# Kernel optimization log

Hardware: AMD Instinct MI355X
Metric: run time of the kernel (lower is better)

## Reference

```python
import jax, jax.numpy as jnp
import numpy as np

D_MODEL = 768
NHEAD = 12
HEAD_DIM = D_MODEL // NHEAD
B, L = 8, 1024


def setup_inputs() -> dict:
    key = jax.random.key(0)
    ks = jax.random.split(key, 10)
    s = 0.02  # init scale for weights
    return {
        "x": jax.random.normal(ks[0], (B, L, D_MODEL), dtype=jnp.float32),
        "pos": jax.random.normal(ks[1], (B, L, D_MODEL), dtype=jnp.float32),
        "qkv_w": jax.random.normal(ks[2], (3 * D_MODEL, D_MODEL), dtype=jnp.float32) * s,
        "qkv_b": jnp.zeros((3 * D_MODEL,), dtype=jnp.float32),
        "pq_w": jax.random.normal(ks[3], (D_MODEL, D_MODEL), dtype=jnp.float32) * s,
        "pq_b": jnp.zeros((D_MODEL,), dtype=jnp.float32),
        "pk_w": jax.random.normal(ks[4], (D_MODEL, D_MODEL), dtype=jnp.float32) * s,
        "pk_b": jnp.zeros((D_MODEL,), dtype=jnp.float32),
    }


def reference(x, pos, qkv_w, qkv_b, pq_w, pq_b, pk_w, pk_b):
    b, l, d = x.shape
    h, hd = NHEAD, HEAD_DIM

    qkv = x @ qkv_w.T + qkv_b  # (b, l, 3d)
    q, k, v = jnp.split(qkv, 3, axis=-1)
    # rearrange 'b l (h d) -> b l h d'
    q = q.reshape(b, l, h, hd)
    k = k.reshape(b, l, h, hd)
    v = v.reshape(b, l, h, hd)

    pq = (pos @ pq_w.T + pq_b).reshape(b, l, h, hd)
    pk = (pos @ pk_w.T + pk_b).reshape(b, l, h, hd)

    CC = jnp.einsum('bnhd,blhd->bhnl', q, k)
    CP = jnp.einsum('bnhd,blhd->bhnl', q, pq)
    PC = jnp.einsum('bnhd,blhd->bhnl', k, pk)

    # Faithful to source: only PC is scaled (operator precedence in original)
    scale = (3 * d) ** 0.5
    attn = jax.nn.softmax(CC + CP + PC / scale, axis=-1)

    out = jnp.einsum('bhnl,blhd->bnhd', attn, v)  # (b, n, h, hd)
    return out
```

## Files before the change

### kernel.cpp

```cpp
#include <hip/hip_runtime.h>
#include <hip/hip_bf16.h>

#define NHEAD 12
#define BATCH 8
#define SEQ 1024
#define LOG2E 1.4426950408889634f

typedef __bf16 bf16x8 __attribute__((ext_vector_type(8)));
typedef float  f32x4  __attribute__((ext_vector_type(4)));

#define WAITVM0 asm volatile("s_waitcnt vmcnt(0)" ::: "memory")
#define WAITVM4 asm volatile("s_waitcnt vmcnt(4)" ::: "memory")

#define MFMA(A, B, C) __builtin_amdgcn_mfma_f32_16x16x32_bf16(A, B, C, 0, 0, 0)

__device__ __forceinline__ unsigned short f2bf(float f) {
    union { float f; unsigned u; } v; v.f = f;
    unsigned u = v.u;
    u += 0x7fff + ((u >> 16) & 1);
    return (unsigned short)(u >> 16);
}

__device__ __forceinline__ unsigned pkbf(float a, float b) {
    union { __hip_bfloat162 h; unsigned u; } cv;
    cv.h = __float22bfloat162_rn(make_float2(a, b));
    return cv.u;
}

__device__ __forceinline__ void gload_lds16(const void* g, void* l) {
    __builtin_amdgcn_global_load_lds(
        (const __attribute__((address_space(1))) unsigned*)g,
        (__attribute__((address_space(3))) unsigned*)l, 16, 0, 0);
}

#define SZ_X    6291456
#define SZ_QKVW 1769472
#define SZ_PW   589824
#define CONV_TOTAL 15532032

__global__ __launch_bounds__(256) void convert_kernel(
    const float* __restrict__ x, const float* __restrict__ pos,
    const float* __restrict__ qkv_w, const float* __restrict__ pq_w,
    const float* __restrict__ pk_w, unsigned short* __restrict__ dst)
{
    const size_t i4 = ((size_t)blockIdx.x * 256 + threadIdx.x) * 4;
    if (i4 >= CONV_TOTAL) return;
    const float* src; size_t off;
    if (i4 < SZ_X)                { src = x;     off = i4; }
    else if (i4 < 2 * SZ_X)       { src = pos;   off = i4 - SZ_X; }
    else if (i4 < 2 * SZ_X + SZ_QKVW) { src = qkv_w; off = i4 - 2 * SZ_X; }
    else if (i4 < 2 * SZ_X + SZ_QKVW + SZ_PW) { src = pq_w; off = i4 - 2 * SZ_X - SZ_QKVW; }
    else                          { src = pk_w;  off = i4 - 2 * SZ_X - SZ_QKVW - SZ_PW; }
    float4 v = *(const float4*)(src + off);
    ushort4 o;
    o.x = f2bf(v.x); o.y = f2bf(v.y); o.z = f2bf(v.z); o.w = f2bf(v.w);
    *(ushort4*)(dst + i4) = o;
}


#define PROJ_STAGE(K0, AS, BS) do {                                          \
    const int k0_ = (K0);                                                    \
    const unsigned short* asrc_; int acol_;                                  \
    if (g == 4)                    { asrc_ = posb; acol_ = k0_; }            \
    else if (g == 3 && k0_ >= 768) { asrc_ = posb; acol_ = k0_ - 768; }      \
    else                           { asrc_ = xb;   acol_ = k0_; }            \
    gload_lds16(asrc_ + (size_t)(m0 + r0) * 768 + acol_ + q0 * 8, &AS[base0]);\
    gload_lds16(asrc_ + (size_t)(m0 + r1) * 768 + acol_ + q1 * 8, &AS[base1]);\
    const unsigned short* wsrc_; int wro_, wco_;                             \
    if (g <= 2)       { wsrc_ = qkvw; wro_ = n0;        wco_ = k0_; }        \
    else if (g == 3) {                                                       \
        if (k0_ < 768) { wsrc_ = qkvw; wro_ = n0 - 1536; wco_ = k0_; }       \
        else           { wsrc_ = pqw;  wro_ = n0 - 2304; wco_ = k0_ - 768; } \
    } else            { wsrc_ = pkw;  wro_ = n0 - 3072; wco_ = k0_; }        \
    gload_lds16(wsrc_ + (size_t)(wro_ + r0) * 768 + wco_ + q0 * 8, &BS[base0]);\
    gload_lds16(wsrc_ + (size_t)(wro_ + r1) * 768 + wco_ + q1 * 8, &BS[base1]);\
} while (0)

#define PROJ_COMPUTE(AS, BS) do {                                            \
    bf16x8 af[4], bfr[4];                                                    \
    _Pragma("unroll")                                                        \
    for (int mt = 0; mt < 4; ++mt) {                                         \
        const int rr = wm + mt * 16 + col16;                                 \
        af[mt] = *(const bf16x8*)&AS[rr * 32 + ((quad ^ ((rr >> 1) & 3)) * 8)];\
    }                                                                        \
    _Pragma("unroll")                                                        \
    for (int nt = 0; nt < 4; ++nt) {                                         \
        const int rr = wn + nt * 16 + col16;                                 \
        bfr[nt] = *(const bf16x8*)&BS[rr * 32 + ((quad ^ ((rr >> 1) & 3)) * 8)];\
    }                                                                        \
    _Pragma("unroll")                                                        \
    for (int mt = 0; mt < 4; ++mt)                                           \
        _Pragma("unroll")                                                    \
        for (int nt = 0; nt < 4; ++nt)                                       \
            acc[mt][nt] = MFMA(af[mt], bfr[nt], acc[mt][nt]);                \
} while (0)

__global__ __launch_bounds__(256, 3) void proj_kernel(
    const unsigned short* __restrict__ xb, const unsigned short* __restrict__ posb,
    const unsigned short* __restrict__ qkvw, const unsigned short* __restrict__ pqw,
    const unsigned short* __restrict__ pkw,
    const float* __restrict__ qkv_b, const float* __restrict__ pq_b,
    const float* __restrict__ pk_b,
    unsigned short* __restrict__ Q2, unsigned short* __restrict__ K2,
    unsigned short* __restrict__ Vt, int band)
{
    __shared__ unsigned short As0[128 * 32];
    __shared__ unsigned short As1[128 * 32];
    __shared__ unsigned short As2[128 * 32];
    __shared__ unsigned short Bs0[128 * 32];
    __shared__ unsigned short Bs1[128 * 32];
    __shared__ unsigned short Bs2[128 * 32];

    const int id  = blockIdx.x;
    const int xcd = id & 7;
    const int idx = id >> 3;
    const int nt30 = (idx / band + 18) % 30;
    const int m0 = (xcd * band + idx % band) * 128;
    const int n0 = nt30 * 128;
    const int g  = n0 / 768;
    const int nk = (g == 3) ? 48 : 24;

    const int tid   = threadIdx.x;
    const int lane  = tid & 63;
    const int w     = tid >> 6;
    const int wm    = (w & 1) * 64;
    const int wn    = (w >> 1) * 64;
    const int quad  = lane >> 4;
    const int col16 = lane & 15;

    const int c0 = w * 64 + lane;
    const int c1 = c0 + 256;
    const int r0 = c0 >> 2, q0 = (c0 & 3) ^ ((c0 >> 3) & 3);
    const int r1 = c1 >> 2, q1 = (c1 & 3) ^ ((c1 >> 3) & 3);
    const int base0 = (w * 64) * 8;
    const int base1 = (w * 64 + 256) * 8;

    f32x4 acc[4][4];
    const f32x4 fzero = {0.f, 0.f, 0.f, 0.f};
#pragma unroll
    for (int mt = 0; mt < 4; ++mt)
#pragma unroll
        for (int nt = 0; nt < 4; ++nt) acc[mt][nt] = fzero;

    PROJ_STAGE(0, As0, Bs0);
    PROJ_STAGE(32, As1, Bs1);

    for (int kt = 0; kt < nk; kt += 3) {
        WAITVM4;
        __syncthreads();
        PROJ_STAGE((kt + 2) * 32, As2, Bs2);
        PROJ_COMPUTE(As0, Bs0);

        WAITVM4;
        __syncthreads();
        if (kt + 3 < nk) PROJ_STAGE((kt + 3) * 32, As0, Bs0);
        PROJ_COMPUTE(As1, Bs1);

        if (kt + 3 >= nk) { WAITVM0; } else { WAITVM4; }
        __syncthreads();
        if (kt + 4 < nk) PROJ_STAGE((kt + 4) * 32, As1, Bs1);
        PROJ_COMPUTE(As2, Bs2);
    }

    if (g == 2) {
#pragma unroll
        for (int mt = 0; mt < 4; ++mt) {
            const int mbase = m0 + wm + mt * 16 + quad * 4;
#pragma unroll
            for (int nt = 0; nt < 4; ++nt) {
                const int n = n0 + wn + nt * 16 + col16;
                const int b = mbase >> 10, l0 = mbase & 1023;
                const int c = n - 1536, h = c >> 6, dd = c & 63;
                const float bias = qkv_b[n];
                uint2 pk;
                pk.x = pkbf(acc[mt][nt][0] + bias, acc[mt][nt][1] + bias);
                pk.y = pkbf(acc[mt][nt][2] + bias, acc[mt][nt][3] + bias);
                *(uint2*)&Vt[((size_t)(b * NHEAD + h) * 64 + dd) * 1024 + l0] = pk;
            }
        }
    } else {
#pragma unroll
        for (int p = 0; p < 4; ++p) {
            __syncthreads();
            if ((wm >> 6) == (p >> 1)) {
#pragma unroll
                for (int mth = 0; mth < 2; ++mth) {
                    const int mt = ((p & 1) << 1) | mth;
#pragma unroll
                    for (int nt = 0; nt < 4; ++nt) {
                        const int n = n0 + wn + nt * 16 + col16;
                        float badd, bmul;
                        if (g == 0)      { badd = qkv_b[n];                         bmul = LOG2E; }
                        else if (g == 1) { badd = qkv_b[n];                         bmul = LOG2E / 48.0f; }
                        else if (g == 3) { badd = qkv_b[n - 1536] + pq_b[n - 2304]; bmul = 1.0f; }
                        else             { badd = pk_b[n - 3072];                   bmul = 1.0f; }
                        const int lrb  = mth * 16 + quad * 4;
                        const int ccol = wn + nt * 16 + col16;
#pragma unroll
                        for (int r = 0; r < 4; ++r)
                            As0[(lrb + r) * 128 + ccol] =
                                f2bf((acc[mt][nt][r] + badd) * bmul);
                    }
                }
            }
            __syncthreads();
#pragma unroll
            for (int j = 0; j < 2; ++j) {
                const int u = tid + 256 * j;
                const int rowp = u >> 4;
                const int seg  = u & 15;
                const int m = m0 + p * 32 + rowp;
                const int b = m >> 10, l = m & 1023;
                const int n = n0 + seg * 8;
                uint4 v = *(const uint4*)&As0[rowp * 128 + seg * 8];
                unsigned short* dst;
                if (g == 0)      { const int h = n >> 6, dd = n & 63;
                                   dst = &Q2[((size_t)(b * NHEAD + h) * 1024 + l) * 128 + dd]; }
                else if (g == 1) { const int c = n - 768,  h = c >> 6, dd = c & 63;
                                   dst = &Q2[((size_t)(b * NHEAD + h) * 1024 + l) * 128 + 64 + dd]; }
                else if (g == 3) { const int c = n - 2304, h = c >> 6, dd = c & 63;
                                   dst = &K2[((size_t)(b * NHEAD + h) * 1024 + l) * 128 + dd]; }
                else             { const int c = n - 3072, h = c >> 6, dd = c & 63;
                                   dst = &K2[((size_t)(b * NHEAD + h) * 1024 + l) * 128 + 64 + dd]; }
                *(uint4*)dst = v;
            }
        }
    }
}


#define ATTN_STG(J0, KS, VS) do {                                            \
    const int j0_ = (J0);                                                    \
    gload_lds16(&K2[q2base + (size_t)(j0_ + kr0) * 128 + kc0 * 8], &KS[kbase0]);\
    gload_lds16(&K2[q2base + (size_t)(j0_ + kr1) * 128 + kc1 * 8], &KS[kbase1]);\
    gload_lds16(&Vt[vtbase + (size_t)vr * 1024 + j0_ + vc * 8],    &VS[vbase]);\
} while (0)

#define ATTN_PV(VS, PSR) do {                                                \
    bf16x8 bp0 = *(const bf16x8*)&PSR[w][col16][quad * 8];                   \
    bf16x8 bp1 = *(const bf16x8*)&PSR[w][16 + col16][quad * 8];              \
    _Pragma("unroll")                                                        \
    for (int c2 = 0; c2 < 4; ++c2) {                                         \
        const int rv = c2 * 16 + col16;                                      \
        bf16x8 av = *(const bf16x8*)&VS[rv * 32 + ((quad ^ ((rv >> 2) & 3)) * 8)];\
        o[0][c2] = MFMA(av, bp0, o[0][c2]);                                  \
        o[1][c2] = MFMA(av, bp1, o[1][c2]);                                  \
    }                                                                        \
} while (0)

#define ATTN_QK(KS, PSW) do {                                                \
    f32x4 st[2][2] = {{fzero, fzero}, {fzero, fzero}};                       \
    _Pragma("unroll")                                                        \
    for (int kk = 0; kk < 4; ++kk) {                                         \
        const int rrj0 = col16, rrj1 = 16 + col16;                           \
        bf16x8 kf0 = *(const bf16x8*)&KS[rrj0 * 128 + (((kk * 4 + quad) ^ (rrj0 & 15)) * 8)];\
        bf16x8 kf1 = *(const bf16x8*)&KS[rrj1 * 128 + (((kk * 4 + quad) ^ (rrj1 & 15)) * 8)];\
        _Pragma("unroll")                                                    \
        for (int qt = 0; qt < 2; ++qt) {                                     \
            st[0][qt] = MFMA(kf0, bq[qt][kk], st[0][qt]);                    \
            st[1][qt] = MFMA(kf1, bq[qt][kk], st[1][qt]);                    \
        }                                                                    \
    }                                                                        \
    _Pragma("unroll")                                                        \
    for (int qt = 0; qt < 2; ++qt) {                                         \
        float p0[4], p1[4], s = 0.f;                                         \
        _Pragma("unroll")                                                    \
        for (int r = 0; r < 4; ++r) {                                        \
            p0[r] = __builtin_amdgcn_exp2f(st[0][qt][r]);                    \
            p1[r] = __builtin_amdgcn_exp2f(st[1][qt][r]);                    \
            s += p0[r] + p1[r];                                              \
        }                                                                    \
        lsum[qt] += s;                                                       \
        uint2 w0, w1;                                                        \
        w0.x = pkbf(p0[0], p0[1]); w0.y = pkbf(p0[2], p0[3]);                \
        w1.x = pkbf(p1[0], p1[1]); w1.y = pkbf(p1[2], p1[3]);                \
        *(uint2*)&PSW[w][qt * 16 + col16][quad * 4]      = w0;               \
        *(uint2*)&PSW[w][qt * 16 + col16][16 + quad * 4] = w1;               \
    }                                                                        \
} while (0)

#define ATTN_PHASE(J, KQK, KST, VPV, VST, PSW, PSR, DOPV, DOST) do {         \
    WAITVM0;                                                                 \
    __syncthreads();                                                         \
    if (DOST) ATTN_STG(((J) + 1) * 32, KST, VST);                            \
    if (DOPV) ATTN_PV(VPV, PSR);                                             \
    ATTN_QK(KQK, PSW);                                                       \
} while (0)

__global__ __launch_bounds__(256, 3) void attn_kernel(
    const unsigned short* __restrict__ Q2, const unsigned short* __restrict__ K2,
    const unsigned short* __restrict__ Vt, float* __restrict__ out, int b0)
{
    __shared__ unsigned short K2sA[32 * 128];
    __shared__ unsigned short K2sB[32 * 128];
    __shared__ unsigned short VtX[64 * 32];
    __shared__ unsigned short VtY[64 * 32];
    __shared__ unsigned short VtZ[64 * 32];
    __shared__ unsigned short Ps0[4][32][40];
    __shared__ unsigned short Ps1[4][32][40];

    const int bh_l = blockIdx.x;
    const int b = b0 + bh_l / NHEAD, h = bh_l % NHEAD;
    const int tid   = threadIdx.x;
    const int lane  = tid & 63;
    const int w     = tid >> 6;
    const int quad  = lane >> 4;
    const int col16 = lane & 15;
    const int qbase = blockIdx.y * 128 + w * 32;

    const size_t q2base = (size_t)bh_l * 1024 * 128;
    const size_t vtbase = (size_t)bh_l * 64 * 1024;

    const int kL0 = w * 64 + lane, kL1 = kL0 + 256;
    const int kr0 = kL0 >> 4, kc0 = (kL0 & 15) ^ (kr0 & 15);
    const int kr1 = kL1 >> 4, kc1 = (kL1 & 15) ^ (kr1 & 15);
    const int vL  = w * 64 + lane;
    const int vr  = vL >> 2,  vc  = (vL & 3) ^ ((vL >> 4) & 3);
    const int kbase0 = (w * 64) * 8, kbase1 = (w * 64 + 256) * 8;
    const int vbase  = (w * 64) * 8;

    bf16x8 bq[2][4];
#pragma unroll
    for (int qt = 0; qt < 2; ++qt)
#pragma unroll
        for (int kk = 0; kk < 4; ++kk)
            bq[qt][kk] = *(const bf16x8*)&Q2[q2base +
                (size_t)(qbase + qt * 16 + col16) * 128 + kk * 32 + quad * 8];

    f32x4 o[2][4];
    const f32x4 fzero = {0.f, 0.f, 0.f, 0.f};
#pragma unroll
    for (int qt = 0; qt < 2; ++qt)
#pragma unroll
        for (int c2 = 0; c2 < 4; ++c2) o[qt][c2] = fzero;
    float lsum[2] = {0.f, 0.f};

    ATTN_STG(0, K2sA, VtX);

    ATTN_PHASE(0, K2sA, K2sB, VtZ, VtY, Ps0, Ps1, 0, 1);

    for (int j = 1; j < 31; j += 6) {
        ATTN_PHASE(j + 0, K2sB, K2sA, VtX, VtZ, Ps1, Ps0, 1, 1);
        ATTN_PHASE(j + 1, K2sA, K2sB, VtY, VtX, Ps0, Ps1, 1, 1);
        ATTN_PHASE(j + 2, K2sB, K2sA, VtZ, VtY, Ps1, Ps0, 1, 1);
        ATTN_PHASE(j + 3, K2sA, K2sB, VtX, VtZ, Ps0, Ps1, 1, 1);
        ATTN_PHASE(j + 4, K2sB, K2sA, VtY, VtX, Ps1, Ps0, 1, 1);
        ATTN_PHASE(j + 5, K2sA, K2sB, VtZ, VtY, Ps0, Ps1, 1, 1);
    }

    ATTN_PHASE(31, K2sB, K2sA, VtX, VtZ, Ps1, Ps0, 1, 0);

    ATTN_PV(VtY, Ps1);

#pragma unroll
    for (int qt = 0; qt < 2; ++qt) {
        lsum[qt] += __shfl_xor(lsum[qt], 16, 64);
        lsum[qt] += __shfl_xor(lsum[qt], 32, 64);
    }

#pragma unroll
    for (int qt = 0; qt < 2; ++qt) {
        const float inv = 1.0f / lsum[qt];
        const int q = qbase + qt * 16 + col16;
#pragma unroll
        for (int c2 = 0; c2 < 4; ++c2) {
#pragma unroll
            for (int r = 0; r < 4; ++r) {
                const int dd = c2 * 16 + quad * 4 + r;
                out[(((size_t)(b * 1024 + q)) * 12 + h) * 64 + dd] = o[qt][c2][r] * inv;
            }
        }
    }
}

extern "C" void kernel_launch(void* const* d_in, const int* in_sizes, int n_in,
                              void* d_out, int out_size, void* d_ws, size_t ws_size,
                              hipStream_t stream) {
    const float* x     = (const float*)d_in[0];
    const float* pos   = (const float*)d_in[1];
    const float* qkv_w = (const float*)d_in[2];
    const float* qkv_b = (const float*)d_in[3];
    const float* pq_w  = (const float*)d_in[4];
    const float* pq_b  = (const float*)d_in[5];
    const float* pk_w  = (const float*)d_in[6];
    const float* pk_b  = (const float*)d_in[7];
    float* out = (float*)d_out;

    unsigned short* ws   = (unsigned short*)d_ws;
    unsigned short* xb   = ws;
    unsigned short* posb = xb + SZ_X;
    unsigned short* qkvw = posb + SZ_X;
    unsigned short* pqw  = qkvw + SZ_QKVW;
    unsigned short* pkw  = pqw + SZ_PW;
    unsigned short* cbuf = pkw + SZ_PW;

    const size_t conv_bytes = (size_t)CONV_TOTAL * 2;
    const size_t per_batch  = (size_t)NHEAD * 1024 * 128 * 4
                            + (size_t)NHEAD * 64 * 1024 * 2;
    int cb = BATCH;
    while (cb > 1 && conv_bytes + (size_t)cb * per_batch > ws_size) cb >>= 1;

    unsigned short* Q2 = cbuf;
    unsigned short* K2 = Q2 + (size_t)cb * NHEAD * 1024 * 128;
    unsigned short* Vt = K2 + (size_t)cb * NHEAD * 1024 * 128;

    convert_kernel<<<(CONV_TOTAL / 4 + 255) / 256, 256, 0, stream>>>(
        x, pos, qkv_w, pq_w, pk_w, ws);

    for (int b0 = 0; b0 < BATCH; b0 += cb) {
        proj_kernel<<<dim3(cb * 240), 256, 0, stream>>>(
            xb + (size_t)b0 * 1024 * 768, posb + (size_t)b0 * 1024 * 768,
            qkvw, pqw, pkw, qkv_b, pq_b, pk_b, Q2, K2, Vt, cb);
        attn_kernel<<<dim3(cb * NHEAD, 8), 256, 0, stream>>>(Q2, K2, Vt, out, b0);
    }
}
```

Before: 234.1 us.

## Load projection A operand directly from global memory, drop A LDS staging

```diff
diff --git a/kernel.cpp b/kernel.cpp
--- a/kernel.cpp
+++ b/kernel.cpp
@@ -10,7 +10,7 @@
 typedef float  f32x4  __attribute__((ext_vector_type(4)));
 
 #define WAITVM0 asm volatile("s_waitcnt vmcnt(0)" ::: "memory")
-#define WAITVM4 asm volatile("s_waitcnt vmcnt(4)" ::: "memory")
+#define WAITVM2 asm volatile("s_waitcnt vmcnt(2)" ::: "memory")
 
 #define MFMA(A, B, C) __builtin_amdgcn_mfma_f32_16x16x32_bf16(A, B, C, 0, 0, 0)
 
@@ -58,14 +58,8 @@
 }
 
 
-#define PROJ_STAGE(K0, AS, BS) do {                                          \
+#define PROJ_STGB(K0, BS) do {                                               \
     const int k0_ = (K0);                                                    \
-    const unsigned short* asrc_; int acol_;                                  \
-    if (g == 4)                    { asrc_ = posb; acol_ = k0_; }            \
-    else if (g == 3 && k0_ >= 768) { asrc_ = posb; acol_ = k0_ - 768; }      \
-    else                           { asrc_ = xb;   acol_ = k0_; }            \
-    gload_lds16(asrc_ + (size_t)(m0 + r0) * 768 + acol_ + q0 * 8, &AS[base0]);\
-    gload_lds16(asrc_ + (size_t)(m0 + r1) * 768 + acol_ + q1 * 8, &AS[base1]);\
     const unsigned short* wsrc_; int wro_, wco_;                             \
     if (g <= 2)       { wsrc_ = qkvw; wro_ = n0;        wco_ = k0_; }        \
     else if (g == 3) {                                                       \
@@ -76,12 +70,17 @@
     gload_lds16(wsrc_ + (size_t)(wro_ + r1) * 768 + wco_ + q1 * 8, &BS[base1]);\
 } while (0)
 
-#define PROJ_COMPUTE(AS, BS) do {                                            \
+#define PROJ_COMPUTE(K0, BS) do {                                            \
+    const int k0a_ = (K0);                                                   \
+    const unsigned short* asrc_; int acol_;                                  \
+    if (g == 4)                     { asrc_ = posb; acol_ = k0a_; }          \
+    else if (g == 3 && k0a_ >= 768) { asrc_ = posb; acol_ = k0a_ - 768; }    \
+    else                            { asrc_ = xb;   acol_ = k0a_; }          \
     bf16x8 af[4], bfr[4];                                                    \
     _Pragma("unroll")                                                        \
     for (int mt = 0; mt < 4; ++mt) {                                         \
         const int rr = wm + mt * 16 + col16;                                 \
-        af[mt] = *(const bf16x8*)&AS[rr * 32 + ((quad ^ ((rr >> 1) & 3)) * 8)];\
+        af[mt] = *(const bf16x8*)&asrc_[(size_t)(m0 + rr) * 768 + acol_ + quad * 8];\
     }                                                                        \
     _Pragma("unroll")                                                        \
     for (int nt = 0; nt < 4; ++nt) {                                         \
@@ -95,7 +94,7 @@
             acc[mt][nt] = MFMA(af[mt], bfr[nt], acc[mt][nt]);                \
 } while (0)
 
-__global__ __launch_bounds__(256, 3) void proj_kernel(
+__global__ __launch_bounds__(256, 4) void proj_kernel(
     const unsigned short* __restrict__ xb, const unsigned short* __restrict__ posb,
     const unsigned short* __restrict__ qkvw, const unsigned short* __restrict__ pqw,
     const unsigned short* __restrict__ pkw,
@@ -104,9 +103,6 @@
     unsigned short* __restrict__ Q2, unsigned short* __restrict__ K2,
     unsigned short* __restrict__ Vt, int band)
 {
-    __shared__ unsigned short As0[128 * 32];
-    __shared__ unsigned short As1[128 * 32];
-    __shared__ unsigned short As2[128 * 32];
     __shared__ unsigned short Bs0[128 * 32];
     __shared__ unsigned short Bs1[128 * 32];
     __shared__ unsigned short Bs2[128 * 32];
@@ -142,24 +138,24 @@
 #pragma unroll
         for (int nt = 0; nt < 4; ++nt) acc[mt][nt] = fzero;
 
-    PROJ_STAGE(0, As0, Bs0);
-    PROJ_STAGE(32, As1, Bs1);
+    PROJ_STGB(0, Bs0);
+    PROJ_STGB(32, Bs1);
 
     for (int kt = 0; kt < nk; kt += 3) {
-        WAITVM4;
+        WAITVM2;
         __syncthreads();
-        PROJ_STAGE((kt + 2) * 32, As2, Bs2);
-        PROJ_COMPUTE(As0, Bs0);
-
-        WAITVM4;
+        PROJ_STGB((kt + 2) * 32, Bs2);
+        PROJ_COMPUTE(kt * 32, Bs0);
+
+        WAITVM2;
         __syncthreads();
-        if (kt + 3 < nk) PROJ_STAGE((kt + 3) * 32, As0, Bs0);
-        PROJ_COMPUTE(As1, Bs1);
-
-        if (kt + 3 >= nk) { WAITVM0; } else { WAITVM4; }
+        if (kt + 3 < nk) PROJ_STGB((kt + 3) * 32, Bs0);
+        PROJ_COMPUTE((kt + 1) * 32, Bs1);
+
+        if (kt + 3 >= nk) { WAITVM0; } else { WAITVM2; }
         __syncthreads();
-        if (kt + 4 < nk) PROJ_STAGE((kt + 4) * 32, As1, Bs1);
-        PROJ_COMPUTE(As2, Bs2);
+        if (kt + 4 < nk) PROJ_STGB((kt + 4) * 32, Bs1);
+        PROJ_COMPUTE((kt + 2) * 32, Bs2);
     }
 
     if (g == 2) {
@@ -198,7 +194,7 @@
                         const int ccol = wn + nt * 16 + col16;
 #pragma unroll
                         for (int r = 0; r < 4; ++r)
-                            As0[(lrb + r) * 128 + ccol] =
+                            Bs0[(lrb + r) * 128 + ccol] =
                                 f2bf((acc[mt][nt][r] + badd) * bmul);
                     }
                 }
@@ -212,7 +208,7 @@
                 const int m = m0 + p * 32 + rowp;
                 const int b = m >> 10, l = m & 1023;
                 const int n = n0 + seg * 8;
-                uint4 v = *(const uint4*)&As0[rowp * 128 + seg * 8];
+                uint4 v = *(const uint4*)&Bs0[rowp * 128 + seg * 8];
                 unsigned short* dst;
                 if (g == 0)      { const int h = n >> 6, dd = n & 63;
                                    dst = &Q2[((size_t)(b * NHEAD + h) * 1024 + l) * 128 + dd]; }
```

New measurement: 285.0 us. +21.8%, slower.
